# Performance work log

Measured on AMD Instinct MI355X. Metric: run time of the kernel, lower is better.

## Reference

```python
import jax, jax.numpy as jnp
import numpy as np
from jax import lax

PAD = 2       # kernel_size=5 -> pad=2
DT = 0.1
NLAYERS = 3

def _circ_pad(x, p=PAD):
    # F.pad(..., mode='circular') on H,W
    return jnp.pad(x, ((0, 0), (0, 0), (p, p), (p, p)), mode='wrap')

def _conv(x, w):
    # torch Conv2d semantics (cross-correlation), NCHW/OIHW, valid padding
    return lax.conv_general_dilated(x, w, (1, 1), 'VALID',
                                    dimension_numbers=('NCHW', 'OIHW', 'NCHW'))

def _gradient(U, K1_w, K2_w):
    # k1 = relu(K1(U)) with circular padding: [B,2,H,W]
    k1 = jax.nn.relu(_conv(_circ_pad(U), K1_w))
    # lam = K2.weight * k1, K2_w shape (1,2,1,1) broadcasts over B,H,W
    lam = K2_w * k1
    # conv_transpose2d(circ_pad(lam), K1_w, padding=4, stride=1)
    # == valid conv with channel-swapped, spatially flipped kernel (k-1-4 = 0 extra pad)
    wT = jnp.transpose(jnp.flip(K1_w, (2, 3)), (1, 0, 2, 3))  # (1,2,5,5)
    return _conv(_circ_pad(lam), wT)  # [B,1,H,W]

def setup_inputs() -> dict:
    key = jax.random.key(0)
    kU, k1, kA = jax.random.split(key, 3)
    B, H, W = 16, 1024, 1024
    U = jax.random.normal(kU, (B, 1, H, W), jnp.float32)
    K1_w = jax.random.normal(k1, (2, 1, 5, 5), jnp.float32) * 0.2
    K2_w = jnp.ones((1, 2, 1, 1), jnp.float32)  # source sets K2 weight to ones
    A_w = jax.random.normal(kA, (1, 1, 5, 5), jnp.float32) * 0.2
    return {"U": U, "K1_w": K1_w, "K2_w": K2_w, "A_w": A_w}

def reference(U, K1_w, K2_w, A_w):
    # explicit Euler: U <- U + dt/nlayers * A(gradient(U)), repeated nlayers times
    for _ in range(NLAYERS):
        grad = _gradient(U, K1_w, K2_w)
        vec = _conv(_circ_pad(grad), A_w)  # self.A (circular conv 1->1)
        U = U + (DT / NLAYERS) * vec
    return U
```

## Files before the change

kernel.cpp:

```cpp
#include <hip/hip_runtime.h>

#define HH 1024
#define WW 1024
#define BH 64
#define DTC (0.1f/3.0f)
#define NSTEP 80

__global__ __launch_bounds__(1024, 4) void pde_band(
    const float* __restrict__ Uin,
    const float* __restrict__ K1,
    const float* __restrict__ K2,
    const float* __restrict__ Aw,
    float* __restrict__ Uout)
{
    __shared__ float shU[2][WW];
    __shared__ float shL[2][2][WW];
    __shared__ float shG[2][WW];

    const int c  = threadIdx.x;
    const int by = blockIdx.x * BH;
    const size_t plane = (size_t)blockIdx.y * (size_t)(HH * WW);
    const float* __restrict__ Ub = Uin + plane;
    float* __restrict__ Ob = Uout + plane;

    float w0[25], w1[25], aw[25];
#pragma unroll
    for (int t = 0; t < 25; ++t) { w0[t] = K1[t]; w1[t] = K1[25 + t]; aw[t] = Aw[t]; }
    const float k2a = K2[0], k2b = K2[1];

    const int cm2 = (c - 2) & (WW - 1), cm1 = (c - 1) & (WW - 1);
    const int cp1 = (c + 1) & (WW - 1), cp2 = (c + 2) & (WW - 1);

    float pL0[5] = {0,0,0,0,0}, pL1[5] = {0,0,0,0,0};
    float pG[5]  = {0,0,0,0,0}, pV[5]  = {0,0,0,0,0};
    float uPrev = 0.f, lPrev0 = 0.f, lPrev1 = 0.f, gPrev = 0.f;

    shU[1][c] = 0.f; shL[1][0][c] = 0.f; shL[1][1][c] = 0.f; shG[1][c] = 0.f;

    float uNew = Ub[(size_t)((unsigned)(by - 6)  & (HH - 1)) * WW + c];
    float idv  = Ub[(size_t)((unsigned)(by - 15) & (HH - 1)) * WW + c];

    for (int sb = 0; sb < NSTEP / 10; ++sb) {
#pragma unroll
      for (int p = 0; p < 10; ++p) {
        const int s   = sb * 10 + p;
        const int p5  = p % 5;
        const int wsl = p & 1;
        const int rsl = wsl ^ 1;
        __syncthreads();

        float uf[5];
        uf[0] = shU[rsl][cm2]; uf[1] = shU[rsl][cm1]; uf[2] = uPrev;
        uf[3] = shU[rsl][cp1]; uf[4] = shU[rsl][cp2];
#pragma unroll
        for (int t = 0; t < 5; ++t) {
          const int sl = (p5 + t) % 5;
#pragma unroll
          for (int j = 0; j < 5; ++j) {
            pL0[sl] = fmaf(uf[j], w0[(4 - t) * 5 + j], pL0[sl]);
            pL1[sl] = fmaf(uf[j], w1[(4 - t) * 5 + j], pL1[sl]);
          }
        }
        const float l0 = fmaxf(pL0[p5], 0.f) * k2a;
        const float l1 = fmaxf(pL1[p5], 0.f) * k2b;
        pL0[p5] = 0.f; pL1[p5] = 0.f;
        shL[wsl][0][c] = l0; shL[wsl][1][c] = l1;

        float lf0[5], lf1[5];
        lf0[0] = shL[rsl][0][cm2]; lf0[1] = shL[rsl][0][cm1]; lf0[2] = lPrev0;
        lf0[3] = shL[rsl][0][cp1]; lf0[4] = shL[rsl][0][cp2];
        lf1[0] = shL[rsl][1][cm2]; lf1[1] = shL[rsl][1][cm1]; lf1[2] = lPrev1;
        lf1[3] = shL[rsl][1][cp1]; lf1[4] = shL[rsl][1][cp2];
#pragma unroll
        for (int t = 0; t < 5; ++t) {
          const int sl = (p5 + t) % 5;
#pragma unroll
          for (int j = 0; j < 5; ++j) {
            pG[sl] = fmaf(lf0[j], w0[t * 5 + 4 - j], pG[sl]);
            pG[sl] = fmaf(lf1[j], w1[t * 5 + 4 - j], pG[sl]);
          }
        }
        const float g = pG[p5]; pG[p5] = 0.f;
        shG[wsl][c] = g;

        float gf[5];
        gf[0] = shG[rsl][cm2]; gf[1] = shG[rsl][cm1]; gf[2] = gPrev;
        gf[3] = shG[rsl][cp1]; gf[4] = shG[rsl][cp2];
#pragma unroll
        for (int t = 0; t < 5; ++t) {
          const int sl = (p5 + t) % 5;
#pragma unroll
          for (int j = 0; j < 5; ++j)
            pV[sl] = fmaf(gf[j], aw[(4 - t) * 5 + j], pV[sl]);
        }
        const float v = pV[p5]; pV[p5] = 0.f;
        if (s >= 15 && s <= 78)
          Ob[(size_t)(by + s - 15) * WW + c] = idv + DTC * v;

        shU[wsl][c] = uNew;
        uPrev = uNew; lPrev0 = l0; lPrev1 = l1; gPrev = g;
        uNew = Ub[(size_t)((unsigned)(by - 5 + s)  & (HH - 1)) * WW + c];
        idv  = Ub[(size_t)((unsigned)(by - 14 + s) & (HH - 1)) * WW + c];
      }
    }
}

extern "C" void kernel_launch(void* const* d_in, const int* in_sizes, int n_in,
                              void* d_out, int out_size, void* d_ws, size_t ws_size,
                              hipStream_t stream) {
    const float* U  = (const float*)d_in[0];
    const float* K1 = (const float*)d_in[1];
    const float* K2 = (const float*)d_in[2];
    const float* Aw = (const float*)d_in[3];
    float* out = (float*)d_out;
    float* ws  = (float*)d_ws;

    const int B = in_sizes[0] / (HH * WW);
    dim3 grid(HH / BH, B);

    pde_band<<<grid, 1024, 0, stream>>>(U,   K1, K2, Aw, out);
    pde_band<<<grid, 1024, 0, stream>>>(out, K1, K2, Aw, ws);
    pde_band<<<grid, 1024, 0, stream>>>(ws,  K1, K2, Aw, out);
}
```

Measured before the change: 308.0 us.

## Process four rows per pipeline step with float4 shared-memory staging

Restructures the row-streaming pipeline so each step handles four rows at once, storing them as float4 in shared memory and using an 8-slot rolling accumulator. This cuts the number of barriers and shared-memory round trips per row, and lets each neighbour load fetch four rows in one access. The cost is more registers per thread and longer per-step latency at 1024 threads per block. The extra warmup steps from the coarser granularity also add some redundant halo work.

```diff
diff --git a/kernel.cpp b/kernel.cpp
--- a/kernel.cpp
+++ b/kernel.cpp
@@ -3,8 +3,8 @@
 #define HH 1024
 #define WW 1024
 #define BH 64
+#define NSTEP 22
 #define DTC (0.1f/3.0f)
-#define NSTEP 80
 
 __global__ __launch_bounds__(1024, 4) void pde_band(
     const float* __restrict__ Uin,
@@ -13,9 +13,10 @@
     const float* __restrict__ Aw,
     float* __restrict__ Uout)
 {
-    __shared__ float shU[2][WW];
-    __shared__ float shL[2][2][WW];
-    __shared__ float shG[2][WW];
+    __shared__ float4 shU [WW];
+    __shared__ float4 shL0[WW];
+    __shared__ float4 shL1[WW];
+    __shared__ float4 shG [WW];
 
     const int c  = threadIdx.x;
     const int by = blockIdx.x * BH;
@@ -31,76 +32,140 @@
     const int cm2 = (c - 2) & (WW - 1), cm1 = (c - 1) & (WW - 1);
     const int cp1 = (c + 1) & (WW - 1), cp2 = (c + 2) & (WW - 1);
 
-    float pL0[5] = {0,0,0,0,0}, pL1[5] = {0,0,0,0,0};
-    float pG[5]  = {0,0,0,0,0}, pV[5]  = {0,0,0,0,0};
-    float uPrev = 0.f, lPrev0 = 0.f, lPrev1 = 0.f, gPrev = 0.f;
+    float pL0[8], pL1[8], pG[8], pV[8];
+#pragma unroll
+    for (int i = 0; i < 8; ++i) { pL0[i]=0.f; pL1[i]=0.f; pG[i]=0.f; pV[i]=0.f; }
 
-    shU[1][c] = 0.f; shL[1][0][c] = 0.f; shL[1][1][c] = 0.f; shG[1][c] = 0.f;
+    float uC[4]  = {0,0,0,0};
+    float lC0[4] = {0,0,0,0};
+    float lC1[4] = {0,0,0,0};
+    float gC[4]  = {0,0,0,0};
 
-    float uNew = Ub[(size_t)((unsigned)(by - 6)  & (HH - 1)) * WW + c];
-    float idv  = Ub[(size_t)((unsigned)(by - 15) & (HH - 1)) * WW + c];
+    const float4 z4 = {0.f, 0.f, 0.f, 0.f};
+    shU[c] = z4; shL0[c] = z4; shL1[c] = z4; shG[c] = z4;
+    __syncthreads();
 
-    for (int sb = 0; sb < NSTEP / 10; ++sb) {
+    for (int sb = 0; sb < NSTEP / 2; ++sb) {
 #pragma unroll
-      for (int p = 0; p < 10; ++p) {
-        const int s   = sb * 10 + p;
-        const int p5  = p % 5;
-        const int wsl = p & 1;
-        const int rsl = wsl ^ 1;
+      for (int p = 0; p < 2; ++p) {
+        const int s = 2 * sb + p;
+
+        float uS[4], idv[4];
+#pragma unroll
+        for (int q = 0; q < 4; ++q) {
+          uS[q]  = Ub[(size_t)((unsigned)(by - 6  + 4*s + q) & (HH-1)) * WW + c];
+          idv[q] = Ub[(size_t)((unsigned)(by - 24 + 4*s + q) & (HH-1)) * WW + c];
+        }
+
+        float nl0[4], nl1[4];
+        {
+          float4 h0 = shU[cm2], h1 = shU[cm1], h2 = shU[cp1], h3 = shU[cp2];
+#pragma unroll
+          for (int q = 0; q < 4; ++q) {
+            const float uf[5] = {
+              reinterpret_cast<const float*>(&h0)[q],
+              reinterpret_cast<const float*>(&h1)[q],
+              uC[q],
+              reinterpret_cast<const float*>(&h2)[q],
+              reinterpret_cast<const float*>(&h3)[q] };
+#pragma unroll
+            for (int t = 0; t < 5; ++t) {
+              const int sl = (4*p + q + t + 4) & 7;
+#pragma unroll
+              for (int j = 0; j < 5; ++j) {
+                pL0[sl] = fmaf(uf[j], w0[(4-t)*5 + j], pL0[sl]);
+                pL1[sl] = fmaf(uf[j], w1[(4-t)*5 + j], pL1[sl]);
+              }
+            }
+          }
+#pragma unroll
+          for (int k = 0; k < 4; ++k) {
+            const int sl = (4*p + k + 4) & 7;
+            nl0[k] = fmaxf(pL0[sl], 0.f) * k2a;  pL0[sl] = 0.f;
+            nl1[k] = fmaxf(pL1[sl], 0.f) * k2b;  pL1[sl] = 0.f;
+          }
+        }
+
+        float ng[4];
+        {
+          float4 a0 = shL0[cm2], a1 = shL0[cm1], a2 = shL0[cp1], a3 = shL0[cp2];
+          float4 b0 = shL1[cm2], b1 = shL1[cm1], b2 = shL1[cp1], b3 = shL1[cp2];
+#pragma unroll
+          for (int q = 0; q < 4; ++q) {
+            const float lf0[5] = {
+              reinterpret_cast<const float*>(&a0)[q],
+              reinterpret_cast<const float*>(&a1)[q],
+              lC0[q],
+              reinterpret_cast<const float*>(&a2)[q],
+              reinterpret_cast<const float*>(&a3)[q] };
+            const float lf1[5] = {
+              reinterpret_cast<const float*>(&b0)[q],
+              reinterpret_cast<const float*>(&b1)[q],
+              lC1[q],
+              reinterpret_cast<const float*>(&b2)[q],
+              reinterpret_cast<const float*>(&b3)[q] };
+#pragma unroll
+            for (int t = 0; t < 5; ++t) {
+              const int sl = (4*p + q + t + 6) & 7;
+#pragma unroll
+              for (int j = 0; j < 5; ++j) {
+                pG[sl] = fmaf(lf0[j], w0[t*5 + 4 - j], pG[sl]);
+                pG[sl] = fmaf(lf1[j], w1[t*5 + 4 - j], pG[sl]);
+              }
+            }
+          }
+#pragma unroll
+          for (int k = 0; k < 4; ++k) {
+            const int sl = (4*p + k + 6) & 7;
+            ng[k] = pG[sl];  pG[sl] = 0.f;
+          }
+        }
+
+        {
+          float4 g0 = shG[cm2], g1 = shG[cm1], g2 = shG[cp1], g3 = shG[cp2];
+#pragma unroll
+          for (int q = 0; q < 4; ++q) {
+            const float gf[5] = {
+              reinterpret_cast<const float*>(&g0)[q],
+              reinterpret_cast<const float*>(&g1)[q],
+              gC[q],
+              reinterpret_cast<const float*>(&g2)[q],
+              reinterpret_cast<const float*>(&g3)[q] };
+#pragma unroll
+            for (int t = 0; t < 5; ++t) {
+              const int sl = (4*p + q + t) & 7;
+#pragma unroll
+              for (int j = 0; j < 5; ++j)
+                pV[sl] = fmaf(gf[j], aw[(4-t)*5 + j], pV[sl]);
+            }
+          }
+          if (s >= 6) {
+#pragma unroll
+            for (int k = 0; k < 4; ++k) {
+              const int sl = (4*p + k) & 7;
+              const int row = by - 24 + 4*s + k;
+              Ob[(size_t)row * WW + c] = idv[k] + DTC * pV[sl];
+              pV[sl] = 0.f;
+            }
+          } else {
+#pragma unroll
+            for (int k = 0; k < 4; ++k) pV[(4*p + k) & 7] = 0.f;
+          }
+        }
+
         __syncthreads();
 
-        float uf[5];
-        uf[0] = shU[rsl][cm2]; uf[1] = shU[rsl][cm1]; uf[2] = uPrev;
-        uf[3] = shU[rsl][cp1]; uf[4] = shU[rsl][cp2];
+        shU[c]  = make_float4(uS[0], uS[1], uS[2], uS[3]);
+        shL0[c] = make_float4(nl0[0], nl0[1], nl0[2], nl0[3]);
+        shL1[c] = make_float4(nl1[0], nl1[1], nl1[2], nl1[3]);
+        shG[c]  = make_float4(ng[0], ng[1], ng[2], ng[3]);
+
+        __syncthreads();
+
 #pragma unroll
-        for (int t = 0; t < 5; ++t) {
-          const int sl = (p5 + t) % 5;
-#pragma unroll
-          for (int j = 0; j < 5; ++j) {
-            pL0[sl] = fmaf(uf[j], w0[(4 - t) * 5 + j], pL0[sl]);
-            pL1[sl] = fmaf(uf[j], w1[(4 - t) * 5 + j], pL1[sl]);
-          }
+        for (int q = 0; q < 4; ++q) {
+          uC[q] = uS[q]; lC0[q] = nl0[q]; lC1[q] = nl1[q]; gC[q] = ng[q];
         }
-        const float l0 = fmaxf(pL0[p5], 0.f) * k2a;
-        const float l1 = fmaxf(pL1[p5], 0.f) * k2b;
-        pL0[p5] = 0.f; pL1[p5] = 0.f;
-        shL[wsl][0][c] = l0; shL[wsl][1][c] = l1;
-
-        float lf0[5], lf1[5];
-        lf0[0] = shL[rsl][0][cm2]; lf0[1] = shL[rsl][0][cm1]; lf0[2] = lPrev0;
-        lf0[3] = shL[rsl][0][cp1]; lf0[4] = shL[rsl][0][cp2];
-        lf1[0] = shL[rsl][1][cm2]; lf1[1] = shL[rsl][1][cm1]; lf1[2] = lPrev1;
-        lf1[3] = shL[rsl][1][cp1]; lf1[4] = shL[rsl][1][cp2];
-#pragma unroll
-        for (int t = 0; t < 5; ++t) {
-          const int sl = (p5 + t) % 5;
-#pragma unroll
-          for (int j = 0; j < 5; ++j) {
-            pG[sl] = fmaf(lf0[j], w0[t * 5 + 4 - j], pG[sl]);
-            pG[sl] = fmaf(lf1[j], w1[t * 5 + 4 - j], pG[sl]);
-          }
-        }
-        const float g = pG[p5]; pG[p5] = 0.f;
-        shG[wsl][c] = g;
-
-        float gf[5];
-        gf[0] = shG[rsl][cm2]; gf[1] = shG[rsl][cm1]; gf[2] = gPrev;
-        gf[3] = shG[rsl][cp1]; gf[4] = shG[rsl][cp2];
-#pragma unroll
-        for (int t = 0; t < 5; ++t) {
-          const int sl = (p5 + t) % 5;
-#pragma unroll
-          for (int j = 0; j < 5; ++j)
-            pV[sl] = fmaf(gf[j], aw[(4 - t) * 5 + j], pV[sl]);
-        }
-        const float v = pV[p5]; pV[p5] = 0.f;
-        if (s >= 15 && s <= 78)
-          Ob[(size_t)(by + s - 15) * WW + c] = idv + DTC * v;
-
-        shU[wsl][c] = uNew;
-        uPrev = uNew; lPrev0 = l0; lPrev1 = l1; gPrev = g;
-        uNew = Ub[(size_t)((unsigned)(by - 5 + s)  & (HH - 1)) * WW + c];
-        idv  = Ub[(size_t)((unsigned)(by - 14 + s) & (HH - 1)) * WW + c];
       }
     }
 }
```

Measured after the change: 511.1 us. 65.9% more time.
